# Optimization experiments

Hardware: AMD Instinct MI355X
Metric: run time of the kernel (lower is better)

The kernel has to match this reference:

```python
import jax, jax.numpy as jnp
import numpy as np

EMBED = 512
HEADS = 8
DH = EMBED // HEADS  # 64
M = 256              # num_landmarks
ITERS = 6            # pinv iterations
SCALE = DH ** -0.5
RES_K = 33           # lucidrains residual_conv_kernel default


def _layer_norm(x, g, b, eps=1e-5):
    mu = jnp.mean(x, axis=-1, keepdims=True)
    var = jnp.mean((x - mu) ** 2, axis=-1, keepdims=True)
    return (x - mu) / jnp.sqrt(var + eps) * g + b


def _pinv_iter(x, iters=ITERS):
    # Moore-Penrose iterative pseudo-inverse (lucidrains nystrom-attention)
    abs_x = jnp.abs(x)
    denom = jnp.max(abs_x.sum(-1)) * jnp.max(abs_x.sum(-2))
    z = jnp.swapaxes(x, -1, -2) / denom
    I = jnp.eye(x.shape[-1], dtype=x.dtype)
    for _ in range(iters):
        xz = x @ z
        z = 0.25 * z @ (13 * I - xz @ (15 * I - xz @ (7 * I - xz)))
    return z


def _dwconv2d(x, w, b):
    # x: [B,C,H,W], w: [C,1,kh,kw] depthwise, SAME padding (odd kernels == k//2)
    out = jax.lax.conv_general_dilated(x, w, (1, 1), 'SAME',
                                       dimension_numbers=('NCHW', 'OIHW', 'NCHW'),
                                       feature_group_count=x.shape[1])
    return out + b[None, :, None, None]


def _nystrom_attn(x, Wqkv, Wo, bo, res_w):
    # x: [B, n, EMBED]; pad at FRONT so n divisible by M (matches F.pad(..., padding, 0) semantics)
    b, n, _ = x.shape
    pad = (M - n % M) % M
    x = jnp.pad(x, ((0, 0), (pad, 0), (0, 0)))
    npad = n + pad
    qkv = x @ Wqkv.T                               # [b, npad, 3*EMBED]
    q, k, v = jnp.split(qkv, 3, axis=-1)
    to_heads = lambda t: t.reshape(b, npad, HEADS, DH).transpose(0, 2, 1, 3)  # bhnd
    q, k, v = to_heads(q), to_heads(k), to_heads(v)
    q = q * SCALE
    l = npad // M
    q_land = q.reshape(b, HEADS, M, l, DH).mean(3)  # [b,h,M,d]
    k_land = k.reshape(b, HEADS, M, l, DH).mean(3)
    s1 = jnp.einsum('bhnd,bhmd->bhnm', q, k_land)
    s2 = jnp.einsum('bhmd,bhld->bhml', q_land, k_land)
    s3 = jnp.einsum('bhmd,bhnd->bhmn', q_land, k)
    a1 = jax.nn.softmax(s1, -1)
    a2 = jax.nn.softmax(s2, -1)
    a3 = jax.nn.softmax(s3, -1)
    a2_inv = _pinv_iter(a2)
    out = a1 @ (a2_inv @ (a3 @ v))                 # [b,h,npad,d]
    # residual depthwise conv over v: channels=heads, spatial=(npad, DH), kernel (33,1)
    res = jax.lax.conv_general_dilated(v, res_w, (1, 1), 'SAME',
                                       dimension_numbers=('NCHW', 'OIHW', 'NCHW'),
                                       feature_group_count=HEADS)
    out = out + res
    out = out.transpose(0, 2, 1, 3).reshape(b, npad, EMBED)
    out = out @ Wo.T + bo
    return out[:, -n:]                             # drop front padding


def setup_inputs() -> dict:
    key = jax.random.key(0)
    ks = jax.random.split(key, 32)
    s = 0.02
    inp = {}
    inp['data'] = jax.random.normal(ks[0], (4, 4096, 1536), jnp.float32)
    inp['W1'] = jax.random.normal(ks[1], (EMBED, 1536), jnp.float32) * s
    inp['b1'] = jnp.zeros((EMBED,), jnp.float32)
    inp['cls_token'] = jax.random.normal(ks[2], (1, 1, EMBED), jnp.float32)
    for li, base in ((1, 3), (2, 9)):
        inp[f'ln{li}_g'] = jnp.ones((EMBED,), jnp.float32)
        inp[f'ln{li}_b'] = jnp.zeros((EMBED,), jnp.float32)
        inp[f'Wqkv{li}'] = jax.random.normal(ks[base], (3 * EMBED, EMBED), jnp.float32) * s
        inp[f'Wo{li}'] = jax.random.normal(ks[base + 1], (EMBED, EMBED), jnp.float32) * s
        inp[f'bo{li}'] = jnp.zeros((EMBED,), jnp.float32)
        inp[f'res{li}'] = jax.random.normal(ks[base + 2], (HEADS, 1, RES_K, 1), jnp.float32) * s
    inp['pw7'] = jax.random.normal(ks[15], (EMBED, 1, 7, 7), jnp.float32) * s
    inp['pb7'] = jnp.zeros((EMBED,), jnp.float32)
    inp['pw5'] = jax.random.normal(ks[16], (EMBED, 1, 5, 5), jnp.float32) * s
    inp['pb5'] = jnp.zeros((EMBED,), jnp.float32)
    inp['pw3'] = jax.random.normal(ks[17], (EMBED, 1, 3, 3), jnp.float32) * s
    inp['pb3'] = jnp.zeros((EMBED,), jnp.float32)
    inp['lnf_g'] = jnp.ones((EMBED,), jnp.float32)
    inp['lnf_b'] = jnp.zeros((EMBED,), jnp.float32)
    inp['W2'] = jax.random.normal(ks[18], (2, EMBED), jnp.float32) * s
    inp['b2'] = jnp.zeros((2,), jnp.float32)
    return inp


def reference(data, W1, b1, cls_token, ln1_g, ln1_b, Wqkv1, Wo1, bo1, res1,
              ln2_g, ln2_b, Wqkv2, Wo2, bo2, res2,
              pw7, pb7, pw5, pb5, pw3, pb3, lnf_g, lnf_b, W2, b2):
    h = jax.nn.relu(data @ W1.T + b1)              # [B, N, EMBED]
    B, N, C = h.shape
    grid = int(np.ceil(np.sqrt(N)))
    add = grid * grid - N
    if add > 0:
        h = jnp.concatenate([h, h[:, :add]], axis=1)
    cls = jnp.broadcast_to(cls_token, (B, 1, C))
    h = jnp.concatenate([cls, h], axis=1)          # [B, 1+grid^2, C]
    # TransLayer 1
    h = h + _nystrom_attn(_layer_norm(h, ln1_g, ln1_b), Wqkv1, Wo1, bo1, res1)
    # PPEG
    cls_t, feat = h[:, :1], h[:, 1:]
    cnn = feat.transpose(0, 2, 1).reshape(B, C, grid, grid)
    x = _dwconv2d(cnn, pw7, pb7) + cnn + _dwconv2d(cnn, pw5, pb5) + _dwconv2d(cnn, pw3, pb3)
    feat = x.reshape(B, C, grid * grid).transpose(0, 2, 1)
    h = jnp.concatenate([cls_t, feat], axis=1)
    # TransLayer 2
    h = h + _nystrom_attn(_layer_norm(h, ln2_g, ln2_b), Wqkv2, Wo2, bo2, res2)
    h = _layer_norm(h, lnf_g, lnf_b)
    cls_feat = h[:, 0]
    logits = cls_feat @ W2.T + b2
    Y_prob = jax.nn.softmax(logits, -1)
    Y_hat = jnp.argmax(Y_prob, -1)
    return logits, Y_prob, Y_hat
```

## Files before the change

kernel.cpp:

```cpp
#include <hip/hip_runtime.h>
#include <math.h>

#define EMBED 512
#define HEADS 8
#define DH 64
#define MM 256
#define LSEG 17
#define NPAD 4352
#define NTOK 4097
#define N0 4096
#define BATCH 4
#define CIN 1536
#define QSCALE 0.125f
#define BH 32
#define NSEG 17

typedef float fp32x4 __attribute__((ext_vector_type(4)));
typedef short bf16x8 __attribute__((ext_vector_type(8)));
typedef short bf16x4 __attribute__((ext_vector_type(4)));
typedef unsigned short u16;

__device__ __forceinline__ unsigned short f2bf(float f) {
  unsigned int u = __float_as_uint(f);
  u += 0x7fffu + ((u >> 16) & 1u);
  return (unsigned short)(u >> 16);
}
__device__ __forceinline__ float bf2f(unsigned short u) {
  return __uint_as_float((unsigned)u << 16);
}

__device__ __forceinline__ float block_sum(float v, float* red) {
  #pragma unroll
  for (int o = 1; o < 64; o <<= 1) v += __shfl_xor(v, o);
  int lane = threadIdx.x & 63, wid = threadIdx.x >> 6;
  if (lane == 0) red[wid] = v;
  __syncthreads();
  float r = red[0] + red[1] + red[2] + red[3];
  __syncthreads();
  return r;
}
__device__ __forceinline__ float block_max(float v, float* red) {
  #pragma unroll
  for (int o = 1; o < 64; o <<= 1) v = fmaxf(v, __shfl_xor(v, o));
  int lane = threadIdx.x & 63, wid = threadIdx.x >> 6;
  if (lane == 0) red[wid] = v;
  __syncthreads();
  float r = fmaxf(fmaxf(red[0], red[1]), fmaxf(red[2], red[3]));
  __syncthreads();
  return r;
}

__global__ void f2bf_kernel(const float* __restrict__ in, u16* __restrict__ out, int n) {
  int t = (blockIdx.x * 256 + threadIdx.x) * 8;
  if (t >= n) return;
  float4 a = *(const float4*)&in[t];
  float4 b = *(const float4*)&in[t + 4];
  bf16x8 pk;
  pk[0]=(short)f2bf(a.x); pk[1]=(short)f2bf(a.y); pk[2]=(short)f2bf(a.z); pk[3]=(short)f2bf(a.w);
  pk[4]=(short)f2bf(b.x); pk[5]=(short)f2bf(b.y); pk[6]=(short)f2bf(b.z); pk[7]=(short)f2bf(b.w);
  *(bf16x8*)&out[t] = pk;
}

__global__ __launch_bounds__(256) void gemm_abt(
    const u16* __restrict__ A, const u16* __restrict__ W,
    int Mrows, int Ncols, int K, const float* __restrict__ bias,
    float* __restrict__ fout, float* __restrict__ fout2,
    u16* __restrict__ uo0, u16* __restrict__ uo1, u16* __restrict__ uo2,
    int mode)
{
  __shared__ u16 As[64][40];
  __shared__ u16 Ws[128][40];
  int tid = threadIdx.x;
  int lane = tid & 63;
  int wv = tid >> 6;
  int rowBase = blockIdx.y * 64, colBase = blockIdx.x * 128;
  int quad = lane >> 4;
  int l15 = lane & 15;
  int sr = tid >> 2;
  int skc = (tid & 3) * 8;

  fp32x4 acc[8];
  #pragma unroll
  for (int i = 0; i < 8; i++) acc[i] = fp32x4{0,0,0,0};

  for (int kb = 0; kb < K; kb += 32) {
    __syncthreads();
    {
      int grow = rowBase + sr;
      bf16x8 av;
      if (grow < Mrows) av = *(const bf16x8*)&A[(size_t)grow * K + kb + skc];
      else { bf16x8 z = {0,0,0,0,0,0,0,0}; av = z; }
      *(bf16x8*)&As[sr][skc] = av;
    }
    #pragma unroll
    for (int h = 0; h < 2; h++) {
      int r = sr + h * 64;
      *(bf16x8*)&Ws[r][skc] =
          *(const bf16x8*)&W[(size_t)(colBase + r) * K + kb + skc];
    }
    __syncthreads();
    bf16x8 aF = *(const bf16x8*)&As[wv * 16 + l15][quad * 8];
    #pragma unroll
    for (int ct = 0; ct < 8; ct++) {
      bf16x8 bF = *(const bf16x8*)&Ws[ct * 16 + l15][quad * 8];
      acc[ct] = __builtin_amdgcn_mfma_f32_16x16x32_bf16(aF, bF, acc[ct], 0, 0, 0);
    }
  }

  #pragma unroll
  for (int ct = 0; ct < 8; ct++) {
    int col = colBase + ct * 16 + l15;
    #pragma unroll
    for (int i = 0; i < 4; i++) {
      int row = rowBase + wv * 16 + quad * 4 + i;
      if (row >= Mrows) continue;
      float v = acc[ct][i];
      if (mode == 0) {
        v += bias[col];
        v = fmaxf(v, 0.f);
        int b = row / N0, n = row % N0;
        fout[((size_t)b * NTOK + 1 + n) * EMBED + col] = v;
      } else if (mode == 1) {
        int b = row / NPAD, n = row % NPAD;
        int sec = col / EMBED;
        int hh = (col % EMBED) / DH;
        int d = col & 63;
        u16* dst = (sec == 0) ? uo0 : ((sec == 1) ? uo1 : uo2);
        if (sec == 0) v *= QSCALE;
        dst[(((size_t)b * HEADS + hh) * NPAD + n) * DH + d] = f2bf(v);
      } else if (mode == 2) {
        v += bias[col];
        fout[(size_t)row * EMBED + col] += v;
      } else {
        v += bias[col];
        float full = fout[(size_t)row * EMBED + col] + v;
        fout[(size_t)row * EMBED + col] = full;
        int b = row / NTOK, t = row % NTOK;
        if (t > 0) fout2[((size_t)b * N0 + (t - 1)) * EMBED + col] = full;
      }
    }
  }
}

__global__ __launch_bounds__(256) void gemm_nn2(
    const u16* __restrict__ A, const u16* __restrict__ Bc,
    u16* __restrict__ Cr, u16* __restrict__ Cc,
    int Nsize, float beta, float sgn, float gamma)
{
  __shared__ u16 As[64][40];
  __shared__ u16 Bs[64][40];
  int batch = blockIdx.z;
  const u16* Ab = A + (size_t)batch * MM * MM;
  const u16* Bb = Bc + (size_t)batch * MM * Nsize;
  int tid = threadIdx.x;
  int lane = tid & 63, wv = tid >> 6, quad = lane >> 4, l15 = lane & 15;
  int rowBase = blockIdx.y * 64, colBase = blockIdx.x * 64;
  int sr = tid >> 2, skc = (tid & 3) * 8;
  fp32x4 acc[4] = {fp32x4{0,0,0,0}, fp32x4{0,0,0,0}, fp32x4{0,0,0,0}, fp32x4{0,0,0,0}};

  for (int kb = 0; kb < MM; kb += 32) {
    __syncthreads();
    *(bf16x8*)&As[sr][skc] = *(const bf16x8*)&Ab[(size_t)(rowBase + sr) * MM + kb + skc];
    *(bf16x8*)&Bs[sr][skc] = *(const bf16x8*)&Bb[(size_t)(colBase + sr) * MM + kb + skc];
    __syncthreads();
    bf16x8 aF = *(const bf16x8*)&As[wv * 16 + l15][quad * 8];
    #pragma unroll
    for (int ct = 0; ct < 4; ct++) {
      bf16x8 bF = *(const bf16x8*)&Bs[ct * 16 + l15][quad * 8];
      acc[ct] = __builtin_amdgcn_mfma_f32_16x16x32_bf16(aF, bF, acc[ct], 0, 0, 0);
    }
  }

  #pragma unroll
  for (int ct = 0; ct < 4; ct++) {
    int col = colBase + ct * 16 + l15;
    #pragma unroll
    for (int i = 0; i < 4; i++) {
      int row = rowBase + wv * 16 + quad * 4 + i;
      float v = sgn * acc[ct][i];
      if (beta != 0.f) v += beta * bf2f(Ab[(size_t)row * MM + col]);
      v *= gamma;
      u16 o = f2bf(v);
      if (Cr) Cr[(size_t)batch * MM * Nsize + (size_t)row * Nsize + col] = o;
      if (Cc) Cc[(size_t)batch * MM * Nsize + (size_t)col * MM + row] = o;
    }
  }
}

__global__ void cls_kernel(const float* __restrict__ cls, float* __restrict__ h) {
  int t = blockIdx.x * blockDim.x + threadIdx.x;
  if (t >= BATCH * EMBED) return;
  int b = t / EMBED, c = t % EMBED;
  h[(size_t)b * NTOK * EMBED + c] = cls[c];
}

__global__ void zero_pad_kernel(u16* __restrict__ xpad) {
  int t = blockIdx.x * blockDim.x + threadIdx.x;
  const int per = 255 * EMBED;
  if (t >= BATCH * per) return;
  int b = t / per, r = t % per;
  xpad[(size_t)b * NPAD * EMBED + r] = 0;
}

__global__ __launch_bounds__(256) void ln_pad_kernel(
    const float* __restrict__ h, const float* __restrict__ g,
    const float* __restrict__ be, u16* __restrict__ xpad)
{
  __shared__ float red[4];
  int row = blockIdx.x;
  int b = row / NTOK, j = row % NTOK;
  const float* x = h + (size_t)row * EMBED;
  int tid = threadIdx.x;
  float v0 = x[tid], v1 = x[tid + 256];
  float mu = block_sum(v0 + v1, red) * (1.f / 512.f);
  float d0 = v0 - mu, d1 = v1 - mu;
  float var = block_sum(d0 * d0 + d1 * d1, red) * (1.f / 512.f);
  float inv = 1.f / sqrtf(var + 1e-5f);
  u16* o = xpad + ((size_t)b * NPAD + 255 + j) * EMBED;
  o[tid]       = f2bf(d0 * inv * g[tid]       + be[tid]);
  o[tid + 256] = f2bf(d1 * inv * g[tid + 256] + be[tid + 256]);
}

__global__ __launch_bounds__(256) void landmarks_kernel(
    const u16* __restrict__ q, const u16* __restrict__ k,
    float* __restrict__ qland, float* __restrict__ kland)
{
  int bh = blockIdx.y;
  int m = blockIdx.x * 4 + (threadIdx.x >> 6);
  int d = threadIdx.x & 63;
  const u16* qb = q + (size_t)bh * NPAD * DH;
  const u16* kb = k + (size_t)bh * NPAD * DH;
  float sq = 0.f, sk = 0.f;
  int base = m * LSEG;
  #pragma unroll
  for (int t = 0; t < LSEG; t++) {
    sq += bf2f(qb[(size_t)(base + t) * DH + d]);
    sk += bf2f(kb[(size_t)(base + t) * DH + d]);
  }
  qland[((size_t)bh * MM + m) * DH + d] = sq * (1.f / LSEG);
  kland[((size_t)bh * MM + m) * DH + d] = sk * (1.f / LSEG);
}

__global__ __launch_bounds__(256) void s2_softmax_kernel(
    const float* __restrict__ qland, const float* __restrict__ kland,
    u16* __restrict__ a2)
{
  __shared__ float qrow[64];
  __shared__ float red[4];
  int bh = blockIdx.y, m = blockIdx.x, tid = threadIdx.x;
  if (tid < 64) qrow[tid] = qland[((size_t)bh * MM + m) * DH + tid];
  __syncthreads();
  const float* kb = kland + (size_t)bh * MM * DH + (size_t)tid * DH;
  float s = 0.f;
  #pragma unroll 16
  for (int d = 0; d < 64; d++) s += qrow[d] * kb[d];
  float mx = block_max(s, red);
  float e = __expf(s - mx);
  float tot = block_sum(e, red);
  a2[((size_t)bh * MM + m) * MM + tid] = f2bf(e / tot);
}

__global__ void init_denom_kernel(float* __restrict__ denoms) {
  if (threadIdx.x < 2) denoms[threadIdx.x] = 0.f;
}

__global__ __launch_bounds__(256) void denom_kernel(
    const u16* __restrict__ a2, float* __restrict__ denoms)
{
  __shared__ float red[4];
  int bh = blockIdx.x, tid = threadIdx.x;
  const u16* A = a2 + (size_t)bh * MM * MM;
  float rs = 0.f, cs = 0.f;
  for (int j = 0; j < MM; j++) rs += bf2f(A[(size_t)tid * MM + j]);
  for (int i = 0; i < MM; i++) cs += bf2f(A[(size_t)i * MM + tid]);
  float mr = block_max(rs, red);
  float mc = block_max(cs, red);
  if (tid == 0) {
    atomicMax((int*)&denoms[0], __float_as_int(mr));
    atomicMax((int*)&denoms[1], __float_as_int(mc));
  }
}

__global__ __launch_bounds__(256) void z0_trans_kernel(
    const u16* __restrict__ a2, const float* __restrict__ denoms,
    u16* __restrict__ zr, u16* __restrict__ zc)
{
  __shared__ u16 tile[64][72];
  int bh = blockIdx.z, i0 = blockIdx.y * 64, j0 = blockIdx.x * 64;
  int tid = threadIdx.x;
  float inv = 1.f / (denoms[0] * denoms[1]);
  const u16* Ab = a2 + (size_t)bh * MM * MM;
  #pragma unroll
  for (int it = 0; it < 4; it++) {
    int idx = it * 1024 + tid * 4;
    int r = idx >> 6, c = idx & 63;
    bf16x4 v = *(const bf16x4*)&Ab[(size_t)(i0 + r) * MM + j0 + c];
    u16 o[4];
    #pragma unroll
    for (int j = 0; j < 4; j++) o[j] = f2bf(bf2f((unsigned short)v[j]) * inv);
    *(bf16x4*)&zc[(size_t)bh * MM * MM + (size_t)(i0 + r) * MM + j0 + c] = *(bf16x4*)o;
    #pragma unroll
    for (int j = 0; j < 4; j++) tile[c + j][r] = o[j];
  }
  __syncthreads();
  #pragma unroll
  for (int it = 0; it < 4; it++) {
    int idx = it * 1024 + tid * 4;
    int r = idx >> 6, c = idx & 63;
    u16 o[4] = {tile[r][c], tile[r][c + 1], tile[r][c + 2], tile[r][c + 3]};
    *(bf16x4*)&zr[(size_t)bh * MM * MM + (size_t)(j0 + r) * MM + i0 + c] = *(bf16x4*)o;
  }
}

__global__ __launch_bounds__(256) void a3v_part_mfma(
    const float* __restrict__ qland, const u16* __restrict__ k,
    const u16* __restrict__ v, u16* __restrict__ Opart,
    float* __restrict__ mpart, float* __restrict__ lpart)
{
  __shared__ __align__(16) u16 qs[64][40];
  __shared__ __align__(16) u16 ks[256][72];
  __shared__ __align__(16) u16 vt[64][72];
  int tid = threadIdx.x;
  int lane = tid & 63, wv = tid >> 6, quad = lane >> 4, l15 = lane & 15;
  int bh = blockIdx.y;
  int ltile = blockIdx.x & 3;
  int seg = blockIdx.x >> 2;
  int l0 = ltile * 64;
  int key0 = seg * 256;
  const float* qb = qland + (size_t)bh * MM * DH;
  const u16* kb = k + (size_t)bh * NPAD * DH;
  const u16* vb = v + (size_t)bh * NPAD * DH;

  {
    int sr = tid >> 2, dc = (tid & 3) * 16;
    const float4* p = (const float4*)&qb[(size_t)(l0 + sr) * DH + dc];
    float4 v0 = p[0], v1 = p[1], v2 = p[2], v3 = p[3];
    float va[16] = {v0.x,v0.y,v0.z,v0.w, v1.x,v1.y,v1.z,v1.w,
                    v2.x,v2.y,v2.z,v2.w, v3.x,v3.y,v3.z,v3.w};
    bf16x8 p0, p1;
    #pragma unroll
    for (int j = 0; j < 8; j++) { p0[j] = (short)f2bf(va[j]); p1[j] = (short)f2bf(va[8 + j]); }
    *(bf16x8*)&qs[sr][dc] = p0;
    *(bf16x8*)&qs[sr][dc + 8] = p1;
  }
  #pragma unroll
  for (int i = 0; i < 16; i++) {
    int idx = i * 1024 + tid * 4;
    int r = idx >> 6, c = idx & 63;
    *(bf16x4*)&ks[r][c] = *(const bf16x4*)&kb[(size_t)(key0 + r) * DH + c];
  }
  __syncthreads();

  fp32x4 sacc[16];
  #pragma unroll
  for (int ct = 0; ct < 16; ct++) sacc[ct] = fp32x4{0,0,0,0};
  bf16x8 aF0 = *(const bf16x8*)&qs[wv * 16 + l15][quad * 8];
  bf16x8 aF1 = *(const bf16x8*)&qs[wv * 16 + l15][32 + quad * 8];
  #pragma unroll
  for (int ct = 0; ct < 16; ct++) {
    bf16x8 b0 = *(const bf16x8*)&ks[ct * 16 + l15][quad * 8];
    bf16x8 b1 = *(const bf16x8*)&ks[ct * 16 + l15][32 + quad * 8];
    sacc[ct] = __builtin_amdgcn_mfma_f32_16x16x32_bf16(aF0, b0, sacc[ct], 0, 0, 0);
    sacc[ct] = __builtin_amdgcn_mfma_f32_16x16x32_bf16(aF1, b1, sacc[ct], 0, 0, 0);
  }

  float mrow[4], lrow[4];
  #pragma unroll
  for (int i = 0; i < 4; i++) {
    float m = -3.0e38f;
    #pragma unroll
    for (int ct = 0; ct < 16; ct++) m = fmaxf(m, sacc[ct][i]);
    #pragma unroll
    for (int o = 1; o < 16; o <<= 1) m = fmaxf(m, __shfl_xor(m, o));
    float s = 0.f;
    #pragma unroll
    for (int ct = 0; ct < 16; ct++) {
      float e = __expf(sacc[ct][i] - m);
      sacc[ct][i] = e;
      s += e;
    }
    #pragma unroll
    for (int o = 1; o < 16; o <<= 1) s += __shfl_xor(s, o);
    mrow[i] = m;
    lrow[i] = s;
  }
  __syncthreads();
  u16* P = &ks[0][0];
  #pragma unroll
  for (int ct = 0; ct < 16; ct++)
    #pragma unroll
    for (int i = 0; i < 4; i++)
      P[(size_t)(wv * 16 + quad * 4 + i) * 264 + ct * 16 + l15] = f2bf(sacc[ct][i]);
  __syncthreads();

  fp32x4 oacc[4] = {fp32x4{0,0,0,0}, fp32x4{0,0,0,0}, fp32x4{0,0,0,0}, fp32x4{0,0,0,0}};
  int dh = tid & 63, kgrp = tid >> 6;
  for (int ch = 0; ch < 4; ch++) {
    if (ch) __syncthreads();
    {
      int kbase = kgrp * 16;
      #pragma unroll
      for (int g = 0; g < 4; g++) {
        u16 pk[4];
        #pragma unroll
        for (int r = 0; r < 4; r++)
          pk[r] = vb[(size_t)(key0 + ch * 64 + kbase + g * 4 + r) * DH + dh];
        *(bf16x4*)&vt[dh][kbase + g * 4] = *(bf16x4*)pk;
      }
    }
    __syncthreads();
    #pragma unroll
    for (int ks2 = 0; ks2 < 2; ks2++) {
      bf16x8 aP = *(const bf16x8*)&P[(size_t)(wv * 16 + l15) * 264 + ch * 64 + ks2 * 32 + quad * 8];
      #pragma unroll
      for (int ct = 0; ct < 4; ct++) {
        bf16x8 bV = *(const bf16x8*)&vt[ct * 16 + l15][ks2 * 32 + quad * 8];
        oacc[ct] = __builtin_amdgcn_mfma_f32_16x16x32_bf16(aP, bV, oacc[ct], 0, 0, 0);
      }
    }
  }

  size_t base = ((size_t)seg * BH + bh) * MM + l0;
  #pragma unroll
  for (int ct = 0; ct < 4; ct++)
    #pragma unroll
    for (int i = 0; i < 4; i++) {
      int row = wv * 16 + quad * 4 + i;
      Opart[(base + row) * DH + ct * 16 + l15] = f2bf(oacc[ct][i]);
    }
  if (l15 == 0) {
    #pragma unroll
    for (int i = 0; i < 4; i++) {
      int row = wv * 16 + quad * 4 + i;
      mpart[base + row] = mrow[i];
      lpart[base + row] = lrow[i];
    }
  }
}

__global__ __launch_bounds__(256) void a3v_merge_kernel(
    const u16* __restrict__ Opart, const float* __restrict__ mpart,
    const float* __restrict__ lpart, u16* __restrict__ kvT)
{
  int bh = blockIdx.y;
  int lbase = blockIdx.x * 64;
  int d = threadIdx.x & 63, lsub = threadIdx.x >> 6;
  for (int li = lsub; li < 64; li += 4) {
    int lm = lbase + li;
    float M = -3.0e38f;
    #pragma unroll
    for (int s = 0; s < NSEG; s++)
      M = fmaxf(M, mpart[((size_t)s * BH + bh) * MM + lm]);
    float L = 0.f, O = 0.f;
    #pragma unroll
    for (int s = 0; s < NSEG; s++) {
      size_t idx = ((size_t)s * BH + bh) * MM + lm;
      float w = __expf(mpart[idx] - M);
      L += lpart[idx] * w;
      O += bf2f(Opart[idx * DH + d]) * w;
    }
    kvT[((size_t)bh * DH + d) * MM + lm] = f2bf(O / L);
  }
}

__global__ __launch_bounds__(256, 2) void attn1_mfma(
    const u16* __restrict__ q, const float* __restrict__ kland,
    const u16* __restrict__ kv2T, const u16* __restrict__ v,
    const float* __restrict__ resw, u16* __restrict__ attn)
{
  __shared__ __align__(16) u16 qs[64][40];
  __shared__ __align__(16) u16 klp[256][72];
  __shared__ __align__(16) u16 kvs[64][264];
  __shared__ float wsm[33];
  int tid = threadIdx.x;
  int lane = tid & 63, wv = tid >> 6, quad = lane >> 4, l15 = lane & 15;
  int bh = blockIdx.y, b = bh >> 3, hh = bh & 7;
  int n0 = 255 + blockIdx.x * 64;
  const u16* qb  = q + (size_t)bh * NPAD * DH;
  const float* klb = kland + (size_t)bh * MM * DH;
  const u16* kvb = kv2T + (size_t)bh * DH * MM;
  const u16* vb  = v + (size_t)bh * NPAD * DH;
  if (tid < 33) wsm[tid] = resw[hh * 33 + tid];

  {
    int sr = tid >> 2, dc = (tid & 3) * 16;
    int g = n0 + sr; if (g > NPAD - 1) g = NPAD - 1;
    *(bf16x8*)&qs[sr][dc]     = *(const bf16x8*)&qb[(size_t)g * DH + dc];
    *(bf16x8*)&qs[sr][dc + 8] = *(const bf16x8*)&qb[(size_t)g * DH + dc + 8];
  }
  #pragma unroll
  for (int i = 0; i < 16; i++) {
    int idx = i * 1024 + tid * 4;
    int r = idx >> 6, c = idx & 63;
    float4 vv = *(const float4*)&klb[(size_t)r * DH + c];
    bf16x4 pk = { (short)f2bf(vv.x), (short)f2bf(vv.y), (short)f2bf(vv.z), (short)f2bf(vv.w) };
    *(bf16x4*)&klp[r][c] = pk;
  }
  #pragma unroll
  for (int i = 0; i < 8; i++) {
    int idx = i * 2048 + tid * 8;
    int r = idx >> 8, c = idx & 255;
    *(bf16x8*)&kvs[r][c] = *(const bf16x8*)&kvb[(size_t)r * MM + c];
  }
  __syncthreads();

  fp32x4 sacc[16];
  #pragma unroll
  for (int ct = 0; ct < 16; ct++) sacc[ct] = fp32x4{0,0,0,0};
  bf16x8 aF0 = *(const bf16x8*)&qs[wv * 16 + l15][quad * 8];
  bf16x8 aF1 = *(const bf16x8*)&qs[wv * 16 + l15][32 + quad * 8];
  #pragma unroll
  for (int ct = 0; ct < 16; ct++) {
    bf16x8 b0 = *(const bf16x8*)&klp[ct * 16 + l15][quad * 8];
    bf16x8 b1 = *(const bf16x8*)&klp[ct * 16 + l15][32 + quad * 8];
    sacc[ct] = __builtin_amdgcn_mfma_f32_16x16x32_bf16(aF0, b0, sacc[ct], 0, 0, 0);
    sacc[ct] = __builtin_amdgcn_mfma_f32_16x16x32_bf16(aF1, b1, sacc[ct], 0, 0, 0);
  }
  #pragma unroll
  for (int i = 0; i < 4; i++) {
    float m = -3.0e38f;
    #pragma unroll
    for (int ct = 0; ct < 16; ct++) m = fmaxf(m, sacc[ct][i]);
    #pragma unroll
    for (int o = 1; o < 16; o <<= 1) m = fmaxf(m, __shfl_xor(m, o));
    float s = 0.f;
    #pragma unroll
    for (int ct = 0; ct < 16; ct++) {
      float e = __expf(sacc[ct][i] - m);
      sacc[ct][i] = e;
      s += e;
    }
    #pragma unroll
    for (int o = 1; o < 16; o <<= 1) s += __shfl_xor(s, o);
    float inv = 1.f / s;
    #pragma unroll
    for (int ct = 0; ct < 16; ct++) sacc[ct][i] *= inv;
  }
  __syncthreads();
  u16* P = &klp[0][0];
  #pragma unroll
  for (int ct = 0; ct < 16; ct++)
    #pragma unroll
    for (int i = 0; i < 4; i++)
      P[(size_t)(wv * 16 + quad * 4 + i) * 264 + ct * 16 + l15] = f2bf(sacc[ct][i]);
  __syncthreads();

  fp32x4 oacc[4] = {fp32x4{0,0,0,0}, fp32x4{0,0,0,0}, fp32x4{0,0,0,0}, fp32x4{0,0,0,0}};
  #pragma unroll
  for (int ks = 0; ks < 8; ks++) {
    bf16x8 aP = *(const bf16x8*)&P[(size_t)(wv * 16 + l15) * 264 + ks * 32 + quad * 8];
    #pragma unroll
    for (int ct = 0; ct < 4; ct++) {
      bf16x8 bV = *(const bf16x8*)&kvs[ct * 16 + l15][ks * 32 + quad * 8];
      oacc[ct] = __builtin_amdgcn_mfma_f32_16x16x32_bf16(aP, bV, oacc[ct], 0, 0, 0);
    }
  }
  __syncthreads();
  float* osm = (float*)&klp[0][0];
  #pragma unroll
  for (int ct = 0; ct < 4; ct++)
    #pragma unroll
    for (int i = 0; i < 4; i++)
      osm[(size_t)(wv * 16 + quad * 4 + i) * 66 + ct * 16 + l15] = oacc[ct][i];
  float* vwin = (float*)&kvs[0][0];
  #pragma unroll
  for (int i = 0; i < 6; i++) {
    int r = i * 16 + (tid >> 4), c = (tid & 15) * 4;
    int g = n0 - 16 + r;
    float4 vv;
    if (g <= NPAD - 1) {
      bf16x4 bv = *(const bf16x4*)&vb[(size_t)g * DH + c];
      vv.x = bf2f((unsigned short)bv[0]); vv.y = bf2f((unsigned short)bv[1]);
      vv.z = bf2f((unsigned short)bv[2]); vv.w = bf2f((unsigned short)bv[3]);
    } else { vv.x = 0.f; vv.y = 0.f; vv.z = 0.f; vv.w = 0.f; }
    *(float4*)&vwin[r * 68 + c] = vv;
  }
  __syncthreads();
  {
    int c = tid & 63, rg = tid >> 6;
    float w[33];
    #pragma unroll
    for (int t = 0; t < 33; t++) w[t] = wsm[t];
    float a16[16];
    #pragma unroll
    for (int r = 0; r < 16; r++) a16[r] = osm[(size_t)(rg * 16 + r) * 66 + c];
    const float* vcol = &vwin[(size_t)(rg * 16) * 68 + c];
    #pragma unroll
    for (int j = 0; j < 48; j++) {
      float vj = vcol[(size_t)j * 68];
      #pragma unroll
      for (int r = 0; r < 16; r++) {
        int t = j - r;
        if (t >= 0 && t < 33) a16[r] += vj * w[t];
      }
    }
    int rowg = n0 + rg * 16;
    #pragma unroll
    for (int r = 0; r < 16; r++) {
      int n = rowg + r;
      if (n > NPAD - 1) continue;
      attn[((size_t)b * NTOK + (n - 255)) * EMBED + hh * DH + c] = f2bf(a16[r]);
    }
  }
}

__global__ void prep_wcomb_kernel(
    const float* __restrict__ pw7, const float* __restrict__ pw5,
    const float* __restrict__ pw3, const float* __restrict__ pb7,
    const float* __restrict__ pb5, const float* __restrict__ pb3,
    float* __restrict__ wcomb, float* __restrict__ biasc)
{
  int i = blockIdx.x * blockDim.x + threadIdx.x;
  if (i < EMBED * 49) {
    int c = i / 49, tap = i % 49;
    int ky = tap / 7, kx = tap % 7;
    float v = pw7[c * 49 + tap];
    if (ky >= 1 && ky <= 5 && kx >= 1 && kx <= 5) v += pw5[c * 25 + (ky - 1) * 5 + (kx - 1)];
    if (ky >= 2 && ky <= 4 && kx >= 2 && kx <= 4) v += pw3[c * 9 + (ky - 2) * 3 + (kx - 2)];
    if (ky == 3 && kx == 3) v += 1.f;
    wcomb[tap * EMBED + c] = v;
  }
  if (i < EMBED) biasc[i] = pb7[i] + pb5[i] + pb3[i];
}

__global__ __launch_bounds__(256) void dwconv_kernel(
    const float* __restrict__ tmp, const float* __restrict__ wcomb,
    const float* __restrict__ biasc, float* __restrict__ h)
{
  int lane = threadIdx.x & 63;
  int xt = threadIdx.x >> 6;
  int cg = blockIdx.x;
  int y  = blockIdx.y;
  int b  = blockIdx.z;
  int c  = cg * 128 + lane * 2;
  int x0 = xt * 16;
  const float* src = tmp + (size_t)b * N0 * EMBED + c;
  float2 bias = *(const float2*)&biasc[c];
  float2 acc[16];
  #pragma unroll
  for (int i = 0; i < 16; i++) acc[i] = bias;
  #pragma unroll
  for (int r = 0; r < 7; r++) {
    int row = y + r - 3;
    if (row < 0 || row >= 64) continue;
    float2 w2[7];
    #pragma unroll
    for (int kx = 0; kx < 7; kx++)
      w2[kx] = *(const float2*)&wcomb[(size_t)(r * 7 + kx) * EMBED + c];
    float2 win[22];
    #pragma unroll
    for (int j = 0; j < 22; j++) {
      int xx = x0 + j - 3;
      if (xx >= 0 && xx < 64)
        win[j] = *(const float2*)&src[((size_t)row * 64 + xx) * EMBED];
      else { win[j].x = 0.f; win[j].y = 0.f; }
    }
    #pragma unroll
    for (int kx = 0; kx < 7; kx++)
      #pragma unroll
      for (int i = 0; i < 16; i++) {
        acc[i].x += win[i + kx].x * w2[kx].x;
        acc[i].y += win[i + kx].y * w2[kx].y;
      }
  }
  float* dst = h + ((size_t)b * NTOK + 1 + (size_t)y * 64) * EMBED + c;
  #pragma unroll
  for (int i = 0; i < 16; i++)
    *(float2*)&dst[(size_t)(x0 + i) * EMBED] = acc[i];
}

__global__ __launch_bounds__(256) void final_kernel(
    const float* __restrict__ h, const float* __restrict__ g,
    const float* __restrict__ be, const float* __restrict__ W2,
    const float* __restrict__ b2, float* __restrict__ out)
{
  __shared__ float red[4];
  int b = blockIdx.x, tid = threadIdx.x;
  const float* x = h + (size_t)b * NTOK * EMBED;
  float v0 = x[tid], v1 = x[tid + 256];
  float mu = block_sum(v0 + v1, red) * (1.f / 512.f);
  float d0 = v0 - mu, d1 = v1 - mu;
  float var = block_sum(d0 * d0 + d1 * d1, red) * (1.f / 512.f);
  float inv = 1.f / sqrtf(var + 1e-5f);
  float xn0 = d0 * inv * g[tid] + be[tid];
  float xn1 = d1 * inv * g[tid + 256] + be[tid + 256];
  float l0 = block_sum(xn0 * W2[tid] + xn1 * W2[tid + 256], red);
  float l1 = block_sum(xn0 * W2[512 + tid] + xn1 * W2[512 + tid + 256], red);
  if (tid == 0) {
    l0 += b2[0]; l1 += b2[1];
    out[b * 2 + 0] = l0;
    out[b * 2 + 1] = l1;
    float mx = fmaxf(l0, l1);
    float e0 = expf(l0 - mx), e1 = expf(l1 - mx);
    float s = e0 + e1;
    out[8 + b * 2 + 0] = e0 / s;
    out[8 + b * 2 + 1] = e1 / s;
    out[16 + b] = (l1 > l0) ? 1.f : 0.f;
  }
}

extern "C" void kernel_launch(void* const* d_in, const int* in_sizes, int n_in,
                              void* d_out, int out_size, void* d_ws, size_t ws_size,
                              hipStream_t stream)
{
  const float* data = (const float*)d_in[0];
  const float* W1   = (const float*)d_in[1];
  const float* b1   = (const float*)d_in[2];
  const float* cls  = (const float*)d_in[3];
  const float* lng[2]  = {(const float*)d_in[4],  (const float*)d_in[10]};
  const float* lnb[2]  = {(const float*)d_in[5],  (const float*)d_in[11]};
  const float* Wqkv[2] = {(const float*)d_in[6],  (const float*)d_in[12]};
  const float* Wo[2]   = {(const float*)d_in[7],  (const float*)d_in[13]};
  const float* bo[2]   = {(const float*)d_in[8],  (const float*)d_in[14]};
  const float* resw[2] = {(const float*)d_in[9],  (const float*)d_in[15]};
  const float* pw7 = (const float*)d_in[16];
  const float* pb7 = (const float*)d_in[17];
  const float* pw5 = (const float*)d_in[18];
  const float* pb5 = (const float*)d_in[19];
  const float* pw3 = (const float*)d_in[20];
  const float* pb3 = (const float*)d_in[21];
  const float* lnfg = (const float*)d_in[22];
  const float* lnfb = (const float*)d_in[23];
  const float* W2  = (const float*)d_in[24];
  const float* b2  = (const float*)d_in[25];

  float* ws = (float*)d_ws;
  size_t off = 0;
  auto alloc = [&](size_t n) { float* p = ws + off; off += n; return p; };
  float* hbuf   = alloc((size_t)BATCH * NTOK * EMBED);
  float* xpadf  = alloc((size_t)BATCH * NPAD * EMBED);
  float* qbuff  = alloc((size_t)BH * NPAD * DH);
  float* kbuff  = alloc((size_t)BH * NPAD * DH);
  float* vbuff  = alloc((size_t)BH * NPAD * DH);
  float* qland  = alloc((size_t)BH * MM * DH);
  float* kland  = alloc((size_t)BH * MM * DH);
  float* a2f    = alloc((size_t)BH * MM * MM / 2);
  float* zaRf   = alloc((size_t)BH * MM * MM / 2);
  float* zaCf   = alloc((size_t)BH * MM * MM / 2);
  float* zbRf   = alloc((size_t)BH * MM * MM / 2);
  float* zbCf   = alloc((size_t)BH * MM * MM / 2);
  float* xzRf   = alloc((size_t)BH * MM * MM / 2);
  float* xzCf   = alloc((size_t)BH * MM * MM / 2);
  float* t1Cf   = alloc((size_t)BH * MM * MM / 2);
  float* t2Cf   = alloc((size_t)BH * MM * MM / 2);
  float* kvTf   = alloc((size_t)BH * MM * DH / 2);
  float* kv2Tf  = alloc((size_t)BH * MM * DH / 2);
  float* wqkvbf = alloc((size_t)2 * 3 * EMBED * EMBED / 2);
  float* wobf   = alloc((size_t)2 * EMBED * EMBED / 2);
  float* wcomb  = alloc(49 * EMBED);
  float* biasc  = alloc(EMBED);
  float* denoms = alloc(64);
  float* mpart  = alloc((size_t)NSEG * BH * MM);
  float* lpart  = alloc((size_t)NSEG * BH * MM);

  u16* xpadB = (u16*)xpadf;
  u16* qB = (u16*)qbuff;
  u16* kB = (u16*)kbuff;
  u16* vB = (u16*)vbuff;
  u16* a2B = (u16*)a2f;
  u16* zaR = (u16*)zaRf; u16* zaC = (u16*)zaCf;
  u16* zbR = (u16*)zbRf; u16* zbC = (u16*)zbCf;
  u16* xzR = (u16*)xzRf; u16* xzC = (u16*)xzCf;
  u16* t1C = (u16*)t1Cf; u16* t2C = (u16*)t2Cf;
  u16* kvT = (u16*)kvTf; u16* kv2T = (u16*)kv2Tf;
  u16* attnB = xpadB;
  u16* OpartB = zaR;
  u16* databf = (u16*)qbuff;
  u16* W1bf = (u16*)vbuff;
  u16* WqkvB[2] = {(u16*)wqkvbf, (u16*)wqkvbf + (size_t)3 * EMBED * EMBED};
  u16* WoB[2]   = {(u16*)wobf,   (u16*)wobf + (size_t)EMBED * EMBED};
  float* convtmp = qbuff;

  int ndata = BATCH * N0 * CIN;
  f2bf_kernel<<<dim3((ndata / 8 + 255) / 256), 256, 0, stream>>>(data, databf, ndata);
  f2bf_kernel<<<dim3((EMBED * CIN / 8 + 255) / 256), 256, 0, stream>>>(W1, W1bf, EMBED * CIN);
  for (int l = 0; l < 2; l++) {
    f2bf_kernel<<<dim3((3 * EMBED * EMBED / 8 + 255) / 256), 256, 0, stream>>>(Wqkv[l], WqkvB[l], 3 * EMBED * EMBED);
    f2bf_kernel<<<dim3((EMBED * EMBED / 8 + 255) / 256), 256, 0, stream>>>(Wo[l], WoB[l], EMBED * EMBED);
  }

  gemm_abt<<<dim3(EMBED / 128, (BATCH * N0) / 64), 256, 0, stream>>>(
      databf, W1bf, BATCH * N0, EMBED, CIN, b1, hbuf, nullptr, nullptr, nullptr, nullptr, 0);
  cls_kernel<<<dim3((BATCH * EMBED + 255) / 256), 256, 0, stream>>>(cls, hbuf);

  for (int layer = 0; layer < 2; layer++) {
    ln_pad_kernel<<<dim3(BATCH * NTOK), 256, 0, stream>>>(hbuf, lng[layer], lnb[layer], xpadB);
    zero_pad_kernel<<<dim3((BATCH * 255 * EMBED + 255) / 256), 256, 0, stream>>>(xpadB);
    gemm_abt<<<dim3((3 * EMBED) / 128, (BATCH * NPAD) / 64), 256, 0, stream>>>(
        xpadB, WqkvB[layer], BATCH * NPAD, 3 * EMBED, EMBED, nullptr,
        nullptr, nullptr, qB, kB, vB, 1);
    landmarks_kernel<<<dim3(MM / 4, BH), 256, 0, stream>>>(qB, kB, qland, kland);
    s2_softmax_kernel<<<dim3(MM, BH), 256, 0, stream>>>(qland, kland, a2B);
    init_denom_kernel<<<1, 64, 0, stream>>>(denoms);
    denom_kernel<<<dim3(BH), 256, 0, stream>>>(a2B, denoms);

    a3v_part_mfma<<<dim3(4 * NSEG, BH), 256, 0, stream>>>(
        qland, kB, vB, OpartB, mpart, lpart);
    a3v_merge_kernel<<<dim3(MM / 64, BH), 256, 0, stream>>>(OpartB, mpart, lpart, kvT);

    z0_trans_kernel<<<dim3(4, 4, BH), 256, 0, stream>>>(a2B, denoms, zaR, zaC);
    u16 *zinR = zaR, *zinC = zaC, *zoutR = zbR, *zoutC = zbC;
    for (int it = 0; it < 6; it++) {
      gemm_nn2<<<dim3(4, 4, BH), 256, 0, stream>>>(a2B, zinC, xzR, xzC, MM, 0.f, 1.f, 1.f);
      gemm_nn2<<<dim3(4, 4, BH), 256, 0, stream>>>(xzR, xzC, nullptr, t1C, MM, 7.f, -1.f, 1.f);
      gemm_nn2<<<dim3(4, 4, BH), 256, 0, stream>>>(xzR, t1C, nullptr, t2C, MM, 15.f, -1.f, 1.f);
      gemm_nn2<<<dim3(4, 4, BH), 256, 0, stream>>>(zinR, t2C, zoutR, zoutC, MM, 13.f, -1.f, 0.25f);
      u16* t;
      t = zinR; zinR = zoutR; zoutR = t;
      t = zinC; zinC = zoutC; zoutC = t;
    }
    gemm_nn2<<<dim3(1, 4, BH), 256, 0, stream>>>(zinR, kvT, nullptr, kv2T, DH, 0.f, 1.f, 1.f);
    attn1_mfma<<<dim3((NTOK + 63) / 64, BH), 256, 0, stream>>>(
        qB, kland, kv2T, vB, resw[layer], attnB);
    gemm_abt<<<dim3(EMBED / 128, (BATCH * NTOK + 63) / 64), 256, 0, stream>>>(
        attnB, WoB[layer], BATCH * NTOK, EMBED, EMBED, bo[layer], hbuf,
        (layer == 0) ? convtmp : nullptr, nullptr, nullptr, nullptr,
        (layer == 0) ? 3 : 2);

    if (layer == 0) {
      prep_wcomb_kernel<<<dim3((EMBED * 49 + 255) / 256), 256, 0, stream>>>(
          pw7, pw5, pw3, pb7, pb5, pb3, wcomb, biasc);
      dwconv_kernel<<<dim3(4, 64, BATCH), 256, 0, stream>>>(
          convtmp, wcomb, biasc, hbuf);
    }
  }

  final_kernel<<<dim3(BATCH), 256, 0, stream>>>(hbuf, lnfg, lnfb, W2, b2, (float*)d_out);
}
```

Baseline: 1.547 ms.

## Fuse pseudo-inverse iteration chain into one persistent kernel per head

```diff
diff --git a/kernel.cpp b/kernel.cpp
--- a/kernel.cpp
+++ b/kernel.cpp
@@ -142,49 +142,109 @@
   }
 }
 
-__global__ __launch_bounds__(256) void gemm_nn2(
-    const u16* __restrict__ A, const u16* __restrict__ Bc,
-    u16* __restrict__ Cr, u16* __restrict__ Cc,
-    int Nsize, float beta, float sgn, float gamma)
-{
-  __shared__ u16 As[64][40];
-  __shared__ u16 Bs[64][40];
-  int batch = blockIdx.z;
-  const u16* Ab = A + (size_t)batch * MM * MM;
-  const u16* Bb = Bc + (size_t)batch * MM * Nsize;
+__global__ __launch_bounds__(1024) void pinv_chain(
+    const u16* __restrict__ a2, const float* __restrict__ denoms,
+    u16* __restrict__ zaR, u16* __restrict__ zaC,
+    u16* __restrict__ zbR, u16* __restrict__ zbC,
+    u16* __restrict__ xzR, u16* __restrict__ xzC,
+    u16* __restrict__ t1C, u16* __restrict__ t2C,
+    const u16* __restrict__ kvT, u16* __restrict__ kv2T)
+{
+  __shared__ __align__(16) u16 Bs[256][264];
+  int bh = blockIdx.x;
+  size_t moff = (size_t)bh * MM * MM;
+  const u16* a2b = a2 + moff;
   int tid = threadIdx.x;
   int lane = tid & 63, wv = tid >> 6, quad = lane >> 4, l15 = lane & 15;
-  int rowBase = blockIdx.y * 64, colBase = blockIdx.x * 64;
-  int sr = tid >> 2, skc = (tid & 3) * 8;
-  fp32x4 acc[4] = {fp32x4{0,0,0,0}, fp32x4{0,0,0,0}, fp32x4{0,0,0,0}, fp32x4{0,0,0,0}};
-
-  for (int kb = 0; kb < MM; kb += 32) {
+  int row0 = wv * 16;
+  float dinv = 1.f / (denoms[0] * denoms[1]);
+
+  {
+    int g = tid >> 8, t256 = tid & 255;
+    u16 (*tile)[72] = (u16 (*)[72])((u16*)Bs + (size_t)g * 64 * 72);
+    for (int rep = 0; rep < 4; rep++) {
+      int idx4 = rep * 4 + g;
+      int i0 = (idx4 >> 2) * 64, j0 = (idx4 & 3) * 64;
+      #pragma unroll
+      for (int it = 0; it < 4; it++) {
+        int idx = it * 1024 + t256 * 4;
+        int r = idx >> 6, c = idx & 63;
+        bf16x4 v = *(const bf16x4*)&a2b[(size_t)(i0 + r) * MM + j0 + c];
+        u16 o[4];
+        #pragma unroll
+        for (int j = 0; j < 4; j++) o[j] = f2bf(bf2f((unsigned short)v[j]) * dinv);
+        *(bf16x4*)&zaC[moff + (size_t)(i0 + r) * MM + j0 + c] = *(bf16x4*)o;
+        #pragma unroll
+        for (int j = 0; j < 4; j++) tile[c + j][r] = o[j];
+      }
+      __syncthreads();
+      #pragma unroll
+      for (int it = 0; it < 4; it++) {
+        int idx = it * 1024 + t256 * 4;
+        int r = idx >> 6, c = idx & 63;
+        u16 o[4] = {tile[r][c], tile[r][c + 1], tile[r][c + 2], tile[r][c + 3]};
+        *(bf16x4*)&zaR[moff + (size_t)(j0 + r) * MM + i0 + c] = *(bf16x4*)o;
+      }
+      __syncthreads();
+    }
+  }
+  __threadfence();
+
+  auto gemmstep = [&](const u16* Ab, const u16* Bb, u16* Cr, u16* Cc,
+                      int Nsize, float beta, float sgn, float gamma) {
+    for (int i = tid * 8; i < Nsize * MM; i += 8192) {
+      int r = i >> 8, c = i & 255;
+      *(bf16x8*)&Bs[r][c] = *(const bf16x8*)&Bb[(size_t)r * MM + c];
+    }
+    bf16x8 aF[8];
+    #pragma unroll
+    for (int kb = 0; kb < 8; kb++)
+      aF[kb] = *(const bf16x8*)&Ab[(size_t)(row0 + l15) * MM + kb * 32 + quad * 8];
     __syncthreads();
-    *(bf16x8*)&As[sr][skc] = *(const bf16x8*)&Ab[(size_t)(rowBase + sr) * MM + kb + skc];
-    *(bf16x8*)&Bs[sr][skc] = *(const bf16x8*)&Bb[(size_t)(colBase + sr) * MM + kb + skc];
+    int nct = Nsize >> 4;
+    for (int ct = 0; ct < nct; ct += 2) {
+      fp32x4 a0 = fp32x4{0,0,0,0}, a1 = fp32x4{0,0,0,0};
+      #pragma unroll
+      for (int kb = 0; kb < 8; kb++) {
+        bf16x8 b0 = *(const bf16x8*)&Bs[ct * 16 + l15][kb * 32 + quad * 8];
+        bf16x8 b1 = *(const bf16x8*)&Bs[ct * 16 + 16 + l15][kb * 32 + quad * 8];
+        a0 = __builtin_amdgcn_mfma_f32_16x16x32_bf16(aF[kb], b0, a0, 0, 0, 0);
+        a1 = __builtin_amdgcn_mfma_f32_16x16x32_bf16(aF[kb], b1, a1, 0, 0, 0);
+      }
+      #pragma unroll
+      for (int h = 0; h < 2; h++) {
+        fp32x4 ac = h ? a1 : a0;
+        int col = (ct + h) * 16 + l15;
+        u16 o[4];
+        #pragma unroll
+        for (int i2 = 0; i2 < 4; i2++) {
+          int row = row0 + quad * 4 + i2;
+          float v = sgn * ac[i2];
+          if (beta != 0.f) v += beta * bf2f(Ab[(size_t)row * MM + col]);
+          v *= gamma;
+          o[i2] = f2bf(v);
+          if (Cr) Cr[(size_t)row * Nsize + col] = o[i2];
+        }
+        if (Cc) *(bf16x4*)&Cc[(size_t)col * MM + row0 + quad * 4] = *(bf16x4*)o;
+      }
+    }
     __syncthreads();
-    bf16x8 aF = *(const bf16x8*)&As[wv * 16 + l15][quad * 8];
-    #pragma unroll
-    for (int ct = 0; ct < 4; ct++) {
-      bf16x8 bF = *(const bf16x8*)&Bs[ct * 16 + l15][quad * 8];
-      acc[ct] = __builtin_amdgcn_mfma_f32_16x16x32_bf16(aF, bF, acc[ct], 0, 0, 0);
-    }
-  }
-
-  #pragma unroll
-  for (int ct = 0; ct < 4; ct++) {
-    int col = colBase + ct * 16 + l15;
-    #pragma unroll
-    for (int i = 0; i < 4; i++) {
-      int row = rowBase + wv * 16 + quad * 4 + i;
-      float v = sgn * acc[ct][i];
-      if (beta != 0.f) v += beta * bf2f(Ab[(size_t)row * MM + col]);
-      v *= gamma;
-      u16 o = f2bf(v);
-      if (Cr) Cr[(size_t)batch * MM * Nsize + (size_t)row * Nsize + col] = o;
-      if (Cc) Cc[(size_t)batch * MM * Nsize + (size_t)col * MM + row] = o;
-    }
-  }
+    __threadfence();
+  };
+
+  u16 *ziR = zaR + moff, *ziC = zaC + moff, *zoR = zbR + moff, *zoC = zbC + moff;
+  u16 *xR = xzR + moff, *xC = xzC + moff, *t1 = t1C + moff, *t2 = t2C + moff;
+  for (int it = 0; it < 6; it++) {
+    gemmstep(a2b, ziC, xR, xC, MM, 0.f, 1.f, 1.f);
+    gemmstep(xR, xC, nullptr, t1, MM, 7.f, -1.f, 1.f);
+    gemmstep(xR, t1, nullptr, t2, MM, 15.f, -1.f, 1.f);
+    gemmstep(ziR, t2, zoR, zoC, MM, 13.f, -1.f, 0.25f);
+    u16* t;
+    t = ziR; ziR = zoR; zoR = t;
+    t = ziC; ziC = zoC; zoC = t;
+  }
+  gemmstep(ziR, kvT + (size_t)bh * MM * DH, nullptr, kv2T + (size_t)bh * MM * DH,
+           DH, 0.f, 1.f, 1.f);
 }
 
 __global__ void cls_kernel(const float* __restrict__ cls, float* __restrict__ h) {
@@ -278,37 +338,6 @@
   if (tid == 0) {
     atomicMax((int*)&denoms[0], __float_as_int(mr));
     atomicMax((int*)&denoms[1], __float_as_int(mc));
-  }
-}
-
-__global__ __launch_bounds__(256) void z0_trans_kernel(
-    const u16* __restrict__ a2, const float* __restrict__ denoms,
-    u16* __restrict__ zr, u16* __restrict__ zc)
-{
-  __shared__ u16 tile[64][72];
-  int bh = blockIdx.z, i0 = blockIdx.y * 64, j0 = blockIdx.x * 64;
-  int tid = threadIdx.x;
-  float inv = 1.f / (denoms[0] * denoms[1]);
-  const u16* Ab = a2 + (size_t)bh * MM * MM;
-  #pragma unroll
-  for (int it = 0; it < 4; it++) {
-    int idx = it * 1024 + tid * 4;
-    int r = idx >> 6, c = idx & 63;
-    bf16x4 v = *(const bf16x4*)&Ab[(size_t)(i0 + r) * MM + j0 + c];
-    u16 o[4];
-    #pragma unroll
-    for (int j = 0; j < 4; j++) o[j] = f2bf(bf2f((unsigned short)v[j]) * inv);
-    *(bf16x4*)&zc[(size_t)bh * MM * MM + (size_t)(i0 + r) * MM + j0 + c] = *(bf16x4*)o;
-    #pragma unroll
-    for (int j = 0; j < 4; j++) tile[c + j][r] = o[j];
-  }
-  __syncthreads();
-  #pragma unroll
-  for (int it = 0; it < 4; it++) {
-    int idx = it * 1024 + tid * 4;
-    int r = idx >> 6, c = idx & 63;
-    u16 o[4] = {tile[r][c], tile[r][c + 1], tile[r][c + 2], tile[r][c + 3]};
-    *(bf16x4*)&zr[(size_t)bh * MM * MM + (size_t)(j0 + r) * MM + i0 + c] = *(bf16x4*)o;
   }
 }
 
@@ -798,18 +827,9 @@
         qland, kB, vB, OpartB, mpart, lpart);
     a3v_merge_kernel<<<dim3(MM / 64, BH), 256, 0, stream>>>(OpartB, mpart, lpart, kvT);
 
-    z0_trans_kernel<<<dim3(4, 4, BH), 256, 0, stream>>>(a2B, denoms, zaR, zaC);
-    u16 *zinR = zaR, *zinC = zaC, *zoutR = zbR, *zoutC = zbC;
-    for (int it = 0; it < 6; it++) {
-      gemm_nn2<<<dim3(4, 4, BH), 256, 0, stream>>>(a2B, zinC, xzR, xzC, MM, 0.f, 1.f, 1.f);
-      gemm_nn2<<<dim3(4, 4, BH), 256, 0, stream>>>(xzR, xzC, nullptr, t1C, MM, 7.f, -1.f, 1.f);
-      gemm_nn2<<<dim3(4, 4, BH), 256, 0, stream>>>(xzR, t1C, nullptr, t2C, MM, 15.f, -1.f, 1.f);
-      gemm_nn2<<<dim3(4, 4, BH), 256, 0, stream>>>(zinR, t2C, zoutR, zoutC, MM, 13.f, -1.f, 0.25f);
-      u16* t;
-      t = zinR; zinR = zoutR; zoutR = t;
-      t = zinC; zinC = zoutC; zoutC = t;
-    }
-    gemm_nn2<<<dim3(1, 4, BH), 256, 0, stream>>>(zinR, kvT, nullptr, kv2T, DH, 0.f, 1.f, 1.f);
+    pinv_chain<<<dim3(BH), 1024, 0, stream>>>(
+        a2B, denoms, zaR, zaC, zbR, zbC, xzR, xzC, t1C, t2C, kvT, kv2T);
+
     attn1_mfma<<<dim3((NTOK + 63) / 64, BH), 256, 0, stream>>>(
         qB, kland, kv2T, vB, resw[layer], attnB);
     gemm_abt<<<dim3(EMBED / 128, (BATCH * NTOK + 63) / 64), 256, 0, stream>>>(
```

After: 2.603 ms. 1.68x slower.
